# Optimization experiments

Hardware: AMD Instinct MI355X
Metric: run time of the kernel (lower is better)

## Reference

```python
import jax, jax.numpy as jnp
import numpy as np

B, L, DIM = 2, 2048, 512
HEADS, R, W, EH, T = 8, 8, 4, 16, 2
HD = DIM // HEADS  # 64
ROPE_BASE = 10000.0


def _local_window_edges(L, w):
    pos = np.arange(L)
    offs = np.concatenate([np.arange(-w, 0), np.arange(1, w + 1)])
    tg = pos[:, None] + offs[None, :]
    valid = (tg >= 0) & (tg < L)
    ii, _ = np.nonzero(valid)          # row-major, matches torch nonzero order
    return ii.astype(np.int32), tg[valid].astype(np.int32)


def setup_inputs() -> dict:
    key = jax.random.key(0)
    ks = jax.random.split(key, 12)
    sd = 0.02
    edge_i, edge_j = _local_window_edges(L, W)
    inp = {
        "x": jax.random.normal(ks[0], (B, L, DIM), jnp.float32),
        "edge_i": jnp.asarray(edge_i),
        "edge_j": jnp.asarray(edge_j),
        "te_w": jax.random.normal(ks[1], (DIM, DIM), jnp.float32) * sd,
        "te_b": jnp.zeros((DIM,), jnp.float32),
        "a1_w": jax.random.normal(ks[2], (2 * DIM, EH), jnp.float32) * sd,
        "a1_b": jnp.zeros((EH,), jnp.float32),
        "a2_w": jax.random.normal(ks[3], (EH, 1), jnp.float32) * sd,
        "a2_b": jnp.zeros((1,), jnp.float32),
        "l1_w": jax.random.normal(ks[4], (2 * DIM, EH), jnp.float32) * sd,
        "l1_b": jnp.zeros((EH,), jnp.float32),
        "l2_w": jax.random.normal(ks[5], (EH, HEADS * R * HD), jnp.float32) * sd,
        "l2_b": jnp.zeros((HEADS * R * HD,), jnp.float32),
        "step_sizes": jnp.full((T, L), -2.2, jnp.float32),
        "out_w": jax.random.normal(ks[6], (DIM, DIM), jnp.float32) * sd,
        "out_b": jnp.zeros((DIM,), jnp.float32),
    }
    return inp


def _rope_cos_sin(rel_pos):
    # rel_pos: [E] int -> cos/sin [E, HD] (rotate-half convention)
    inv_freq = 1.0 / (ROPE_BASE ** (jnp.arange(0, HD, 2, dtype=jnp.float32) / HD))
    ang = rel_pos.astype(jnp.float32)[:, None] * inv_freq[None, :]  # [E, HD/2]
    ang = jnp.concatenate([ang, ang], axis=-1)                      # [E, HD]
    return jnp.cos(ang), jnp.sin(ang)


def _rotate_half(x):
    x1, x2 = x[..., : HD // 2], x[..., HD // 2:]
    return jnp.concatenate([-x2, x1], axis=-1)


def reference(x, edge_i, edge_j, te_w, te_b, a1_w, a1_b, a2_w, a2_b,
              l1_w, l1_b, l2_w, l2_b, step_sizes, out_w, out_b):
    E = edge_i.shape[0]
    # token encoder -> heads: u [B, H, L, HD]
    u = (x @ te_w + te_b).reshape(B, L, HEADS, HD).transpose(0, 2, 1, 3)

    # edge features from raw x: [B, E, 2*DIM]
    ef = jnp.concatenate([x[:, edge_i], x[:, edge_j]], axis=-1)
    # alpha: softplus MLP -> [B, E]
    h = jax.nn.gelu(ef @ a1_w + a1_b, approximate=False)
    alphas = jax.nn.softplus((h @ a2_w + a2_b)[..., 0])
    # Lambda: MLP -> [B, E, H, R, HD], L2-normalized on last dim
    h2 = jax.nn.gelu(ef @ l1_w + l1_b, approximate=False)
    Lam = (h2 @ l2_w + l2_b).reshape(B, E, HEADS, R, HD)
    Lam = Lam / jnp.maximum(jnp.linalg.norm(Lam, axis=-1, keepdims=True), 1e-12)

    cos, sin = _rope_cos_sin(edge_i - edge_j)  # [E, HD] each

    for t in range(T):
        eta = jax.nn.softplus(step_sizes[t])[None, None, :, None]  # [1,1,L,1]
        u_i = u[:, :, edge_i]                                      # [B,H,E,HD]
        u_j = u[:, :, edge_j]
        u_i = u_i * cos + _rotate_half(u_i) * sin
        diff = u_i - u_j
        ld = jnp.einsum('behrd,bhed->bher', Lam, diff)
        residual = alphas[:, None, :, None] * diff + jnp.einsum('bher,behrd->bhed', ld, Lam)
        upd = jnp.zeros_like(u).at[:, :, edge_i, :].add(residual)
        upd = upd.at[:, :, edge_j, :].add(-residual)
        u = u - eta * upd

    u = u.transpose(0, 2, 1, 3).reshape(B, L, DIM)
    return u @ out_w + out_b
```

## Files before the change

kernel.cpp:

```cpp
#include <hip/hip_runtime.h>
#include <hip/hip_bf16.h>

#define B_   2
#define L_   2048
#define DIM_ 512
#define NH_  8
#define HD_  64
#define R_   8
#define EH_  16
#define T_   2

typedef unsigned int uint32;
typedef unsigned short ushort_t;

__device__ __forceinline__ float gelu_f(float x){
  return 0.5f * x * (1.0f + erff(x * 0.70710678118654752f));
}
__device__ __forceinline__ float softplus_f(float x){
  return (x > 20.f) ? x : log1pf(expf(x));
}
__device__ __forceinline__ constexpr int off_of(int o){ return (o < 4) ? o - 4 : o - 3; }
__device__ __forceinline__ ushort_t fbf(float f){
  uint32 u = __float_as_uint(f);
  return (ushort_t)((u + 0x7FFFu + ((u >> 16) & 1u)) >> 16);
}
__device__ __forceinline__ float blo(uint32 w){ return __uint_as_float(w << 16); }
__device__ __forceinline__ float bhi(uint32 w){ return __uint_as_float(w & 0xFFFF0000u); }

__global__ __launch_bounds__(256) void k_misc(
    const float* __restrict__ l2w, const float* __restrict__ l2b,
    const float* __restrict__ step,
    float* __restrict__ W2, float* __restrict__ eta,
    float* __restrict__ ropeC, float* __restrict__ ropeS,
    int* __restrict__ esrc, int* __restrict__ edst)
{
  int idx = blockIdx.x * 256 + threadIdx.x;
  if (idx < NH_*144*64){
    int d = idx & 63;
    int n = (idx >> 6) % 144;
    int h = idx / (144*64);
    int k = n >> 3, r = n & 7;
    int col = h*512 + r*64 + d;
    float v = 0.f;
    if (k < 16) v = l2w[k*4096 + col];
    else if (k == 16) v = l2b[col];
    W2[idx] = v;
    return;
  }
  idx -= NH_*144*64;
  if (idx < T_*L_){ eta[idx] = softplus_f(step[idx]); return; }
  idx -= T_*L_;
  if (idx < 9*32){
    int d = idx & 31, rel = (idx >> 5) - 4;
    float invf = expf(-((float)d / 32.f) * 9.210340371976184f);
    float ang = (float)rel * invf;
    ropeC[idx] = cosf(ang); ropeS[idx] = sinf(ang);
    return;
  }
  idx -= 9*32;
  if (idx < 2*8*L_){
    if (idx < 8*L_) esrc[idx] = -1; else edst[idx - 8*L_] = -1;
    return;
  }
}

__global__ __launch_bounds__(256) void k_cvtw(
    const float* __restrict__ W2, ushort_t* __restrict__ W2h)
{
  int idx = blockIdx.x * 256 + threadIdx.x;
  if (idx < NH_*144*64) W2h[idx] = fbf(W2[idx]);
}

__global__ __launch_bounds__(256) void k_gram(
    const float* __restrict__ W2, float* __restrict__ Gram)
{
  int idx = blockIdx.x * 256 + threadIdx.x;
  if (idx >= 8*8*17*17) return;
  int bq = idx % 17;
  int a  = (idx / 17) % 17;
  int r  = (idx / 289) & 7;
  int h  = idx / (289*8);
  const float* wa = W2 + ((size_t)(h*144 + a*8 + r))*64;
  const float* wb = W2 + ((size_t)(h*144 + bq*8 + r))*64;
  float s = 0.f;
  #pragma unroll 8
  for (int d = 0; d < 64; d++) s = fmaf(wa[d], wb[d], s);
  Gram[idx] = s;
}

__global__ __launch_bounds__(256) void k_fill(
    const int* __restrict__ ei, const int* __restrict__ ej, int E,
    int* __restrict__ esrc, int* __restrict__ edst)
{
  int e = blockIdx.x * 256 + threadIdx.x;
  if (e >= E) return;
  int i = ei[e], j = ej[e];
  int o = j - i;
  int slot = (o < 0) ? (o + 4) : (o + 3);
  esrc[slot*L_ + i] = e;
  edst[slot*L_ + j] = e;
}

__global__ __launch_bounds__(256) void k_te(
    const float* __restrict__ x, const float* __restrict__ w,
    const float* __restrict__ bias, float* __restrict__ u)
{
  __shared__ float As[16][64];
  __shared__ float Bs[16][64];
  const int m0 = blockIdx.x * 64;
  const int n0 = blockIdx.y * 64;
  const int tid = threadIdx.x;
  const int ty = tid >> 4, tx = tid & 15;
  float acc[4][4] = {};
  for (int k0 = 0; k0 < 512; k0 += 16){
    {
      int m = tid >> 2, seg = tid & 3;
      float4 v = *(const float4*)(x + (size_t)(m0 + m)*512 + k0 + seg*4);
      As[seg*4+0][m] = v.x; As[seg*4+1][m] = v.y;
      As[seg*4+2][m] = v.z; As[seg*4+3][m] = v.w;
    }
    {
      int k = tid >> 4, c = (tid & 15)*4;
      float4 v = *(const float4*)(w + (size_t)(k0 + k)*512 + n0 + c);
      *(float4*)&Bs[k][c] = v;
    }
    __syncthreads();
    #pragma unroll
    for (int k = 0; k < 16; k++){
      float4 a = *(const float4*)(&As[k][ty*4]);
      float4 b = *(const float4*)(&Bs[k][tx*4]);
      float av[4] = {a.x, a.y, a.z, a.w};
      float bv[4] = {b.x, b.y, b.z, b.w};
      #pragma unroll
      for (int ii = 0; ii < 4; ii++)
        #pragma unroll
        for (int jj = 0; jj < 4; jj++)
          acc[ii][jj] = fmaf(av[ii], bv[jj], acc[ii][jj]);
    }
    __syncthreads();
  }
  const int bb = m0 >> 11;
  const int lb = (m0 & 2047) + ty*4;
  #pragma unroll
  for (int jj = 0; jj < 4; jj++){
    int n = n0 + tx*4 + jj;
    float bv = bias[n];
    float4 o;
    o.x = acc[0][jj] + bv; o.y = acc[1][jj] + bv;
    o.z = acc[2][jj] + bv; o.w = acc[3][jj] + bv;
    *(float4*)&u[((size_t)(bb*512 + n))*2048 + lb] = o;
  }
}

__global__ __launch_bounds__(256) void k_pq(
    const float* __restrict__ x, const float* __restrict__ a1w,
    const float* __restrict__ l1w, float* __restrict__ PQ)
{
  __shared__ float As[16][64];
  __shared__ float Bs[16][64];
  const int m0 = blockIdx.x * 64;
  const int tid = threadIdx.x;
  const int ty = tid >> 4, tx = tid & 15;
  const int c = (tid & 15) * 4;
  const int group = c >> 4;
  const float* src = (group & 2) ? l1w : a1w;
  const int krow_off = (group & 1) ? 512 : 0;
  const int cc = c & 15;
  float acc[4][4] = {};
  for (int k0 = 0; k0 < 512; k0 += 16){
    {
      int m = tid >> 2, seg = tid & 3;
      float4 v = *(const float4*)(x + (size_t)(m0 + m)*512 + k0 + seg*4);
      As[seg*4+0][m] = v.x; As[seg*4+1][m] = v.y;
      As[seg*4+2][m] = v.z; As[seg*4+3][m] = v.w;
    }
    {
      int k = tid >> 4;
      float4 v = *(const float4*)(src + (size_t)(krow_off + k0 + k)*16 + cc);
      *(float4*)&Bs[k][c] = v;
    }
    __syncthreads();
    #pragma unroll
    for (int k = 0; k < 16; k++){
      float4 a = *(const float4*)(&As[k][ty*4]);
      float4 b = *(const float4*)(&Bs[k][tx*4]);
      float av[4] = {a.x, a.y, a.z, a.w};
      float bv[4] = {b.x, b.y, b.z, b.w};
      #pragma unroll
      for (int ii = 0; ii < 4; ii++)
        #pragma unroll
        for (int jj = 0; jj < 4; jj++)
          acc[ii][jj] = fmaf(av[ii], bv[jj], acc[ii][jj]);
    }
    __syncthreads();
  }
  #pragma unroll
  for (int ii = 0; ii < 4; ii++){
    int m = m0 + ty*4 + ii;
    float4 o;
    o.x = acc[ii][0]; o.y = acc[ii][1]; o.z = acc[ii][2]; o.w = acc[ii][3];
    *(float4*)&PQ[(size_t)m*64 + tx*4] = o;
  }
}

__global__ __launch_bounds__(256) void k_feat2(
    const float* __restrict__ PQ, const int* __restrict__ ei, const int* __restrict__ ej,
    const float* __restrict__ a1b, const float* __restrict__ a2w,
    const float* __restrict__ a2b, const float* __restrict__ l1b,
    int E, float* __restrict__ alphas, float* __restrict__ h2e,
    float* __restrict__ h2t)
{
  int e = blockIdx.x * 256 + threadIdx.x;
  int b = blockIdx.y;
  if (e >= E) return;
  int i = ei[e], j = ej[e];
  const float* Pi = PQ + ((size_t)b*L_ + i)*64;
  const float* Pj = PQ + ((size_t)b*L_ + j)*64;
  float ha[16], hl[16];
  #pragma unroll
  for (int q = 0; q < 4; q++){
    float4 p1 = *(const float4*)(Pi + q*4);
    float4 q1 = *(const float4*)(Pj + 16 + q*4);
    float4 p2 = *(const float4*)(Pi + 32 + q*4);
    float4 q2 = *(const float4*)(Pj + 48 + q*4);
    ha[q*4+0] = p1.x + q1.x; ha[q*4+1] = p1.y + q1.y;
    ha[q*4+2] = p1.z + q1.z; ha[q*4+3] = p1.w + q1.w;
    hl[q*4+0] = p2.x + q2.x; hl[q*4+1] = p2.y + q2.y;
    hl[q*4+2] = p2.z + q2.z; hl[q*4+3] = p2.w + q2.w;
  }
  float av = a2b[0];
  #pragma unroll
  for (int n = 0; n < 16; n++){
    float g = gelu_f(ha[n] + a1b[n]);
    av += g * a2w[n];
  }
  alphas[(size_t)b*E + e] = softplus_f(av);
  float* he = h2e + ((size_t)b*E + e)*16;
  #pragma unroll
  for (int n = 0; n < 16; n++){
    float g = gelu_f(hl[n] + l1b[n]);
    he[n] = g;
    h2t[((size_t)b*16 + n)*E + e] = g;
  }
}

__global__ __launch_bounds__(256) void k_norm(
    const float* __restrict__ Gram, const float* __restrict__ h2e,
    int E, float* __restrict__ ivsq)
{
  __shared__ float Gl[8*289];
  __shared__ float Hl[256*17];
  const int tid = threadIdx.x;
  const int bh = blockIdx.y;
  const int b = bh >> 3, h = bh & 7;
  const int eb = blockIdx.x*256;
  for (int it = tid; it < 2312; it += 256) Gl[it] = Gram[(size_t)h*2312 + it];
  {
    int ge = eb + tid;
    const float* hp = h2e + ((size_t)b*E + (ge < E ? ge : 0))*16;
    #pragma unroll
    for (int q = 0; q < 4; q++){
      float4 v = *(const float4*)(hp + q*4);
      Hl[tid*17+q*4+0]=v.x; Hl[tid*17+q*4+1]=v.y;
      Hl[tid*17+q*4+2]=v.z; Hl[tid*17+q*4+3]=v.w;
    }
    Hl[tid*17+16] = 1.f;
  }
  __syncthreads();
  int ge = eb + tid;
  if (ge >= E) return;
  float m17[17];
  #pragma unroll
  for (int k = 0; k < 17; k++) m17[k] = Hl[tid*17+k];
  float* ig = ivsq + ((size_t)bh*E + ge)*8;
  #pragma unroll
  for (int r = 0; r < 8; r++){
    float ss = 0.f;
    for (int a = 0; a < 17; a++){
      float ma = Hl[tid*17 + a];
      const float* Gr = Gl + r*289 + a*17;
      float inner = 0.f;
      #pragma unroll
      for (int bq = 0; bq < 17; bq++)
        inner = fmaf(m17[bq], Gr[bq], inner);
      ss = fmaf(ma, inner, ss);
    }
    ig[r] = 1.f / fmaxf(ss, 1e-24f);
  }
}

__global__ __launch_bounds__(256) void k_S(
    const float* __restrict__ u, const ushort_t* __restrict__ W2h,
    const float* __restrict__ h2t,
    const float* __restrict__ ropeC, const float* __restrict__ ropeS,
    const int* __restrict__ ei, const int* __restrict__ ej,
    int E, const float* __restrict__ ivsq, float* __restrict__ coefg)
{
  __shared__ uint32 Wl[136*32];
  __shared__ float rCT[288], rST[288];
  const int tid = threadIdx.x;
  const int bh = blockIdx.y;
  const int b = bh >> 3, h = bh & 7;
  const int eb = blockIdx.x*256;

  {
    const uint4* Wg4 = (const uint4*)(W2h + (size_t)h*144*64);
    for (int fi = tid; fi < 1088; fi += 256)
      ((uint4*)Wl)[fi] = Wg4[fi];
  }
  for (int it = tid; it < 288; it += 256){
    int rix = it >> 5, p = it & 31;
    rCT[p*9 + rix] = ropeC[it];
    rST[p*9 + rix] = ropeS[it];
  }
  __syncthreads();

  const int dq = tid & 3;
  const int qd = tid >> 2;
  const int e0 = eb + qd*4;
  const int p0 = 8*dq;
  const float* ub = u + ((size_t)(b*512 + h*64))*2048;
  const float* h2b = h2t + (size_t)b*16*E;

  int iiv[4], jjv[4], rxv[4];
  #pragma unroll
  for (int s = 0; s < 4; s++){
    int ge = e0 + s;
    int gi = (ge < E) ? ge : (E-1);
    iiv[s] = ei[gi]; jjv[s] = ej[gi];
    rxv[s] = iiv[s] - jjv[s] + 4;
  }

  float dA[4][8], dB[4][8];
  #pragma unroll
  for (int s = 0; s < 4; s++){
    #pragma unroll
    for (int q = 0; q < 8; q++){
      int dp = p0 + q;
      float c  = rCT[dp*9 + rxv[s]];
      float sn = rST[dp*9 + rxv[s]];
      float ui0 = ub[(size_t)dp*2048 + iiv[s]];
      float ui1 = ub[(size_t)(dp+32)*2048 + iiv[s]];
      float uj0 = ub[(size_t)dp*2048 + jjv[s]];
      float uj1 = ub[(size_t)(dp+32)*2048 + jjv[s]];
      dA[s][q] = ui0*c - ui1*sn - uj0;
      dB[s][q] = ui1*c + ui0*sn - uj1;
    }
  }

  const uint4* Wl4 = (const uint4*)Wl;
  float P[4][8] = {};
  for (int k = 0; k < 17; k++){
    float mk0, mk1, mk2, mk3;
    if (k < 16){
      float4 m4 = *(const float4*)(h2b + (size_t)k*E + e0);
      mk0 = m4.x; mk1 = m4.y; mk2 = m4.z; mk3 = m4.w;
    } else {
      mk0 = mk1 = mk2 = mk3 = 1.f;
    }
    const int rowb = (k*8)*8;
    #pragma unroll
    for (int r = 0; r < 8; r++){
      uint4 wa = Wl4[rowb + r*8 + dq];
      uint4 wb = Wl4[rowb + r*8 + 4 + dq];
      #pragma unroll
      for (int s = 0; s < 4; s++){
        float pd;
        pd = dA[s][0]*blo(wa.x);
        pd = fmaf(dA[s][1], bhi(wa.x), pd);
        pd = fmaf(dA[s][2], blo(wa.y), pd);
        pd = fmaf(dA[s][3], bhi(wa.y), pd);
        pd = fmaf(dA[s][4], blo(wa.z), pd);
        pd = fmaf(dA[s][5], bhi(wa.z), pd);
        pd = fmaf(dA[s][6], blo(wa.w), pd);
        pd = fmaf(dA[s][7], bhi(wa.w), pd);
        pd = fmaf(dB[s][0], blo(wb.x), pd);
        pd = fmaf(dB[s][1], bhi(wb.x), pd);
        pd = fmaf(dB[s][2], blo(wb.y), pd);
        pd = fmaf(dB[s][3], bhi(wb.y), pd);
        pd = fmaf(dB[s][4], blo(wb.z), pd);
        pd = fmaf(dB[s][5], bhi(wb.z), pd);
        pd = fmaf(dB[s][6], blo(wb.w), pd);
        pd = fmaf(dB[s][7], bhi(wb.w), pd);
        float mk = (s==0)?mk0:(s==1)?mk1:(s==2)?mk2:mk3;
        P[s][r] = fmaf(mk, pd, P[s][r]);
      }
    }
  }

  #pragma unroll
  for (int s = 0; s < 4; s++)
    #pragma unroll
    for (int r = 0; r < 8; r++){
      float v = P[s][r];
      v += __shfl_xor(v, 1);
      v += __shfl_xor(v, 2);
      P[s][r] = v;
    }

  int ge = e0 + dq;
  if (ge < E){
    float S8[8];
    #pragma unroll
    for (int r = 0; r < 8; r++){
      float v0 = P[0][r], v1 = P[1][r], v2 = P[2][r], v3 = P[3][r];
      S8[r] = (dq==0) ? v0 : (dq==1) ? v1 : (dq==2) ? v2 : v3;
    }
    const float* ig = ivsq + ((size_t)bh*E + ge)*8;
    float* cg = coefg + ((size_t)bh*E + ge)*8;
    #pragma unroll
    for (int r = 0; r < 8; r++) cg[r] = ig[r]*S8[r];
  }
}

__global__ __launch_bounds__(256) void k_apply(
    const float* __restrict__ uin, float* __restrict__ uout,
    const float* __restrict__ W2,
    const float* __restrict__ h2e, const float* __restrict__ coefg,
    const float* __restrict__ alphas,
    const float* __restrict__ ropeC, const float* __restrict__ ropeS,
    const int* __restrict__ esrc, const int* __restrict__ edst,
    const int* __restrict__ ei, const int* __restrict__ ej,
    const float* __restrict__ eta, int E, int t)
{
  __shared__ float smem[10816];
  float* Al  = smem;
  float* UtF = smem;
  float* SaF = smem + 4896;
  int*   Es  = (int*)(smem + 9216);
  float* rCl = smem + 10240;
  float* rSl = smem + 10528;

  const int tid = threadIdx.x;
  const int l0 = blockIdx.x * 64;
  const int bh = blockIdx.y;
  const int b = bh >> 3, h = bh & 7;
  const float* ub = uin + ((size_t)(b*512 + h*64))*2048;
  float*       uo = uout + ((size_t)(b*512 + h*64))*2048;
  const float* Wg = W2 + (size_t)h*144*64;

  #pragma unroll
  for (int it = 0; it < 4; it++){
    int si = it*256 + tid;
    int o = si >> 6, ll = si & 63;
    Es[si] = (o < 8) ? esrc[o*L_ + l0 + ll] : edst[(o-8)*L_ + l0 + ll];
  }
  for (int it = tid; it < 288; it += 256){ rCl[it] = ropeC[it]; rSl[it] = ropeS[it]; }
  for (int it = tid; it < 9216; it += 256) Al[it] = 0.f;
  __syncthreads();

  {
    const int l = tid & 63;
    const int kc = tid >> 6;
    const int kbase = kc*4;
    float areg[5][8];
    #pragma unroll
    for (int k = 0; k < 5; k++)
      #pragma unroll
      for (int r = 0; r < 8; r++) areg[k][r] = 0.f;
    for (int o = 0; o < 16; o++){
      int e = Es[o*64 + l];
      if (e < 0) continue;
      float sign = (o < 8) ? 1.f : -1.f;
      const float* hp = h2e + ((size_t)b*E + e)*16;
      const float* cp = coefg + ((size_t)bh*E + e)*8;
      float4 m4 = *(const float4*)(hp + kbase);
      float4 c0 = *(const float4*)cp;
      float4 c1 = *(const float4*)(cp + 4);
      float cf[8] = {c0.x, c0.y, c0.z, c0.w, c1.x, c1.y, c1.z, c1.w};
      float smv[4] = {sign*m4.x, sign*m4.y, sign*m4.z, sign*m4.w};
      #pragma unroll
      for (int k = 0; k < 4; k++)
        #pragma unroll
        for (int r = 0; r < 8; r++)
          areg[k][r] = fmaf(smv[k], cf[r], areg[k][r]);
      if (kc == 3){
        #pragma unroll
        for (int r = 0; r < 8; r++) areg[4][r] += sign*cf[r];
      }
    }
    const int sw = (l >> 2) & 3;
    #pragma unroll
    for (int k = 0; k < 4; k++){
      #pragma unroll
      for (int r = 0; r < 8; r++){
        int n = (kbase + k)*8 + r;
        Al[l*144 + (((n >> 2) ^ sw) << 2) + (n & 3)] = areg[k][r];
      }
    }
    if (kc == 3){
      #pragma unroll
      for (int r = 0; r < 8; r++){
        int n = 128 + r;
        Al[l*144 + (((n >> 2) ^ sw) << 2) + (n & 3)] = areg[4][r];
      }
    }
  }
  __syncthreads();

  const int lg = tid & 15, dg = tid >> 4;
  float acc[4][4] = {};
  {
    const int swr = lg & 3;
    for (int nf4 = 0; nf4 < 34; nf4++){
      int sf4 = (nf4 ^ swr) << 2;
      float4 Av[4];
      #pragma unroll
      for (int tt = 0; tt < 4; tt++)
        Av[tt] = *(const float4*)&Al[(lg*4 + tt)*144 + sf4];
      int n = nf4*4;
      #pragma unroll
      for (int q = 0; q < 4; q++){
        float4 wb = *(const float4*)(Wg + (size_t)(n + q)*64 + dg*4);
        #pragma unroll
        for (int tt = 0; tt < 4; tt++){
          float a = (q==0)?Av[tt].x:(q==1)?Av[tt].y:(q==2)?Av[tt].z:Av[tt].w;
          acc[tt][0] = fmaf(a, wb.x, acc[tt][0]);
          acc[tt][1] = fmaf(a, wb.y, acc[tt][1]);
          acc[tt][2] = fmaf(a, wb.z, acc[tt][2]);
          acc[tt][3] = fmaf(a, wb.w, acc[tt][3]);
        }
      }
    }
  }
  __syncthreads();

  #pragma unroll
  for (int it = 0; it < 18; it++){
    int flat = it*256 + tid;
    int d = flat / 72;
    int c = flat - d*72;
    int col = l0 - 4 + c;
    col = (col < 0) ? 0 : ((col > 2047) ? 2047 : col);
    UtF[c*68 + d] = ub[(size_t)d*2048 + col];
  }
  #pragma unroll
  for (int it = 0; it < 4; it++){
    int si = it*256 + tid;
    int e = Es[si];
    SaF[si] = (e >= 0) ? alphas[(size_t)b*E + e] : 0.f;
  }
  __syncthreads();

  const int pbase = (dg*4) & 31;
  const float sgn = (dg < 8) ? -1.f : 1.f;
  const int pcol = (dg*4 + 32) & 63;
  float4 rcv[8], rsv[8];
  #pragma unroll
  for (int o = 0; o < 8; o++){
    const int rix = 4 - off_of(o);
    rcv[o] = *(const float4*)&rCl[rix*32 + pbase];
    rsv[o] = *(const float4*)&rSl[rix*32 + pbase];
  }
  #pragma unroll
  for (int tt = 0; tt < 4; tt++){
    const int ll = lg*4 + tt;
    const int myl = l0 + ll;
    const int lrel = ll + 4;
    const float et = eta[t*L_ + myl];
    float4 ul  = *(const float4*)&UtF[lrel*68 + dg*4];
    float4 ulp = *(const float4*)&UtF[lrel*68 + pcol];
    float upd[4] = {acc[tt][0], acc[tt][1], acc[tt][2], acc[tt][3]};
    float ulv[4] = {ul.x, ul.y, ul.z, ul.w};
    float ulpv[4] = {ulp.x, ulp.y, ulp.z, ulp.w};
    #pragma unroll
    for (int o = 0; o < 8; o++){
      int e = Es[o*64 + ll];
      if (e >= 0){
        float al = SaF[o*64 + ll];
        float4 uj = *(const float4*)&UtF[(lrel + off_of(o))*68 + dg*4];
        float ujv[4] = {uj.x, uj.y, uj.z, uj.w};
        float rc[4] = {rcv[o].x, rcv[o].y, rcv[o].z, rcv[o].w};
        float rs[4] = {rsv[o].x, rsv[o].y, rsv[o].z, rsv[o].w};
        #pragma unroll
        for (int q = 0; q < 4; q++){
          float rope = rc[q]*ulv[q] + sgn*rs[q]*ulpv[q];
          upd[q] = fmaf(al, rope - ujv[q], upd[q]);
        }
      }
    }
    #pragma unroll
    for (int o = 0; o < 8; o++){
      int e = Es[(8 + o)*64 + ll];
      if (e >= 0){
        float al = SaF[(8 + o)*64 + ll];
        int lr2 = lrel - off_of(o);
        float4 ui  = *(const float4*)&UtF[lr2*68 + dg*4];
        float4 uip = *(const float4*)&UtF[lr2*68 + pcol];
        float uiv[4] = {ui.x, ui.y, ui.z, ui.w};
        float uipv[4] = {uip.x, uip.y, uip.z, uip.w};
        float rc[4] = {rcv[o].x, rcv[o].y, rcv[o].z, rcv[o].w};
        float rs[4] = {rsv[o].x, rsv[o].y, rsv[o].z, rsv[o].w};
        #pragma unroll
        for (int q = 0; q < 4; q++){
          float rope = rc[q]*uiv[q] + sgn*rs[q]*uipv[q];
          upd[q] -= al * (rope - ulv[q]);
        }
      }
    }
    #pragma unroll
    for (int q = 0; q < 4; q++)
      uo[(size_t)(dg*4 + q)*2048 + myl] = ulv[q] - et*upd[q];
  }
}

__global__ __launch_bounds__(256) void k_out(
    const float* __restrict__ u, const float* __restrict__ w,
    const float* __restrict__ bias, float* __restrict__ outp)
{
  __shared__ float As[16][64];
  __shared__ float Bs[16][64];
  const int m0 = blockIdx.x * 64;
  const int n0 = blockIdx.y * 64;
  const int tid = threadIdx.x;
  const int ty = tid >> 4, tx = tid & 15;
  const int bb = m0 >> 11;
  const int l0 = m0 & 2047;
  float acc[4][4] = {};
  for (int k0 = 0; k0 < 512; k0 += 16){
    {
      int k = tid >> 4, ls = (tid & 15)*4;
      float4 v = *(const float4*)&u[((size_t)(bb*512 + k0 + k))*2048 + l0 + ls];
      *(float4*)&As[k][ls] = v;
    }
    {
      int k = tid >> 4, c = (tid & 15)*4;
      float4 v = *(const float4*)(w + (size_t)(k0 + k)*512 + n0 + c);
      *(float4*)&Bs[k][c] = v;
    }
    __syncthreads();
    #pragma unroll
    for (int k = 0; k < 16; k++){
      float4 a = *(const float4*)(&As[k][ty*4]);
      float4 b = *(const float4*)(&Bs[k][tx*4]);
      float av[4] = {a.x, a.y, a.z, a.w};
      float bv[4] = {b.x, b.y, b.z, b.w};
      #pragma unroll
      for (int ii = 0; ii < 4; ii++)
        #pragma unroll
        for (int jj = 0; jj < 4; jj++)
          acc[ii][jj] = fmaf(av[ii], bv[jj], acc[ii][jj]);
    }
    __syncthreads();
  }
  float bv[4];
  #pragma unroll
  for (int jj = 0; jj < 4; jj++) bv[jj] = bias[n0 + tx*4 + jj];
  #pragma unroll
  for (int ii = 0; ii < 4; ii++){
    int l = l0 + ty*4 + ii;
    float4 o;
    o.x = acc[ii][0] + bv[0];
    o.y = acc[ii][1] + bv[1];
    o.z = acc[ii][2] + bv[2];
    o.w = acc[ii][3] + bv[3];
    *(float4*)&outp[((size_t)(bb*2048 + l))*512 + n0 + tx*4] = o;
  }
}

extern "C" void kernel_launch(void* const* d_in, const int* in_sizes, int n_in,
                              void* d_out, int out_size, void* d_ws, size_t ws_size,
                              hipStream_t stream)
{
  const float* x    = (const float*)d_in[0];
  const int*   ei   = (const int*)d_in[1];
  const int*   ej   = (const int*)d_in[2];
  const float* tew  = (const float*)d_in[3];
  const float* teb  = (const float*)d_in[4];
  const float* a1w  = (const float*)d_in[5];
  const float* a1b  = (const float*)d_in[6];
  const float* a2w  = (const float*)d_in[7];
  const float* a2b  = (const float*)d_in[8];
  const float* l1w  = (const float*)d_in[9];
  const float* l1b  = (const float*)d_in[10];
  const float* l2w  = (const float*)d_in[11];
  const float* l2b  = (const float*)d_in[12];
  const float* step = (const float*)d_in[13];
  const float* ow   = (const float*)d_in[14];
  const float* ob   = (const float*)d_in[15];
  float* outp = (float*)d_out;
  const int E = in_sizes[1];

  char* p = (char*)d_ws;
  auto carve = [&](size_t nbytes)->char*{
    char* q = p; p += (nbytes + 255) & ~(size_t)255; return q;
  };
  float* u0     = (float*)carve((size_t)B_*512*2048*4);
  float* u1     = (float*)carve((size_t)B_*512*2048*4);
  float* PQ     = (float*)carve((size_t)B_*L_*64*4);
  float* h2e    = (float*)carve((size_t)B_*E*16*4);
  float* h2t    = (float*)carve((size_t)(B_*16*E + 64)*4);
  float* alphas = (float*)carve((size_t)B_*E*4);
  float* coefg  = (float*)carve((size_t)B_*NH_*E*8*4);
  float* ivsq   = (float*)carve((size_t)B_*NH_*E*8*4);
  float* W2     = (float*)carve((size_t)NH_*144*64*4);
  ushort_t* W2h = (ushort_t*)carve((size_t)NH_*144*64*2);
  float* Gram   = (float*)carve((size_t)8*8*17*17*4);
  float* eta    = (float*)carve((size_t)T_*L_*4);
  float* ropeC  = (float*)carve((size_t)288*4);
  float* ropeS  = (float*)carve((size_t)288*4);
  int*   esrc   = (int*)carve((size_t)8*L_*4);
  int*   edst   = (int*)carve((size_t)8*L_*4);

  {
    int total = NH_*144*64 + T_*L_ + 9*32 + 2*8*L_;
    k_misc<<<dim3((total + 255)/256), dim3(256), 0, stream>>>(
        l2w, l2b, step, W2, eta, ropeC, ropeS, esrc, edst);
  }
  k_cvtw<<<dim3((NH_*144*64 + 255)/256), dim3(256), 0, stream>>>(W2, W2h);
  k_gram<<<dim3((8*8*17*17 + 255)/256), dim3(256), 0, stream>>>(W2, Gram);
  k_fill<<<dim3((E + 255)/256), dim3(256), 0, stream>>>(ei, ej, E, esrc, edst);
  k_te<<<dim3(64, 8), dim3(256), 0, stream>>>(x, tew, teb, u0);
  k_pq<<<dim3(64), dim3(256), 0, stream>>>(x, a1w, l1w, PQ);
  k_feat2<<<dim3((E + 255)/256, B_), dim3(256), 0, stream>>>(
      PQ, ei, ej, a1b, a2w, a2b, l1b, E, alphas, h2e, h2t);

  k_norm<<<dim3((E + 255)/256, B_*NH_), dim3(256), 0, stream>>>(Gram, h2e, E, ivsq);

  const int etiles = (E + 255)/256;
  float* ucur = u0;
  float* unxt = u1;
  for (int t = 0; t < T_; t++){
    k_S<<<dim3(etiles, B_*NH_), dim3(256), 0, stream>>>(
        ucur, W2h, h2t, ropeC, ropeS, ei, ej, E, ivsq, coefg);
    k_apply<<<dim3(L_/64, B_*NH_), dim3(256), 0, stream>>>(
        ucur, unxt, W2, h2e, coefg, alphas, ropeC, ropeS,
        esrc, edst, ei, ej, eta, E, t);
    float* tmp = ucur; ucur = unxt; unxt = tmp;
  }

  k_out<<<dim3(64, 8), dim3(256), 0, stream>>>(ucur, ow, ob, outp);
}
```

Baseline: 377.9 us.

## Split k_S dot products across 8 lanes with paired bf16 weight layout

The bf16 weight table is repacked so each 32-bit word holds the rotate-half pair (d, d+32), letting one uint4 LDS load feed both halves of the rope-rotated diff. k_S now uses 8 lanes per edge group, each handling 4 of the 32 rotary pairs, instead of 4 lanes with 8 pairs each. Each block therefore covers 128 edges and the grid doubles. This lowers per-thread registers and LDS loads and raises parallelism, at the cost of an extra shuffle-reduction step, idle lanes during the final store, and twice as many block-level weight staging loads.

```diff
diff --git a/kernel.cpp b/kernel.cpp
--- a/kernel.cpp
+++ b/kernel.cpp
@@ -65,10 +65,17 @@
 }
 
 __global__ __launch_bounds__(256) void k_cvtw(
-    const float* __restrict__ W2, ushort_t* __restrict__ W2h)
+    const float* __restrict__ W2, uint32* __restrict__ W2p)
 {
   int idx = blockIdx.x * 256 + threadIdx.x;
-  if (idx < NH_*144*64) W2h[idx] = fbf(W2[idx]);
+  if (idx >= NH_*144*32) return;
+  int dp = idx & 31;
+  int n  = (idx >> 5) % 144;
+  int h  = idx / (144*32);
+  const float* row = W2 + ((size_t)h*144 + n)*64;
+  uint32 lo = fbf(row[dp]);
+  uint32 hi = fbf(row[dp+32]);
+  W2p[idx] = lo | (hi << 16);
 }
 
 __global__ __launch_bounds__(256) void k_gram(
@@ -290,7 +297,7 @@
 }
 
 __global__ __launch_bounds__(256) void k_S(
-    const float* __restrict__ u, const ushort_t* __restrict__ W2h,
+    const float* __restrict__ u, const uint32* __restrict__ W2p,
     const float* __restrict__ h2t,
     const float* __restrict__ ropeC, const float* __restrict__ ropeS,
     const int* __restrict__ ei, const int* __restrict__ ej,
@@ -301,10 +308,10 @@
   const int tid = threadIdx.x;
   const int bh = blockIdx.y;
   const int b = bh >> 3, h = bh & 7;
-  const int eb = blockIdx.x*256;
+  const int eb = blockIdx.x*128;
 
   {
-    const uint4* Wg4 = (const uint4*)(W2h + (size_t)h*144*64);
+    const uint4* Wg4 = (const uint4*)(W2p + (size_t)h*144*32);
     for (int fi = tid; fi < 1088; fi += 256)
       ((uint4*)Wl)[fi] = Wg4[fi];
   }
@@ -315,10 +322,10 @@
   }
   __syncthreads();
 
-  const int dq = tid & 3;
-  const int qd = tid >> 2;
+  const int og = tid & 7;
+  const int qd = tid >> 3;
   const int e0 = eb + qd*4;
-  const int p0 = 8*dq;
+  const int p0 = og*4;
   const float* ub = u + ((size_t)(b*512 + h*64))*2048;
   const float* h2b = h2t + (size_t)b*16*E;
 
@@ -331,11 +338,11 @@
     rxv[s] = iiv[s] - jjv[s] + 4;
   }
 
-  float dA[4][8], dB[4][8];
+  float dA[4][4], dB[4][4];
   #pragma unroll
   for (int s = 0; s < 4; s++){
     #pragma unroll
-    for (int q = 0; q < 8; q++){
+    for (int q = 0; q < 4; q++){
       int dp = p0 + q;
       float c  = rCT[dp*9 + rxv[s]];
       float sn = rST[dp*9 + rxv[s]];
@@ -361,27 +368,22 @@
     const int rowb = (k*8)*8;
     #pragma unroll
     for (int r = 0; r < 8; r++){
-      uint4 wa = Wl4[rowb + r*8 + dq];
-      uint4 wb = Wl4[rowb + r*8 + 4 + dq];
+      uint4 w = Wl4[rowb + r*8 + og];
+      float wa0 = blo(w.x), wb0 = bhi(w.x);
+      float wa1 = blo(w.y), wb1 = bhi(w.y);
+      float wa2 = blo(w.z), wb2 = bhi(w.z);
+      float wa3 = blo(w.w), wb3 = bhi(w.w);
       #pragma unroll
       for (int s = 0; s < 4; s++){
         float pd;
-        pd = dA[s][0]*blo(wa.x);
-        pd = fmaf(dA[s][1], bhi(wa.x), pd);
-        pd = fmaf(dA[s][2], blo(wa.y), pd);
-        pd = fmaf(dA[s][3], bhi(wa.y), pd);
-        pd = fmaf(dA[s][4], blo(wa.z), pd);
-        pd = fmaf(dA[s][5], bhi(wa.z), pd);
-        pd = fmaf(dA[s][6], blo(wa.w), pd);
-        pd = fmaf(dA[s][7], bhi(wa.w), pd);
-        pd = fmaf(dB[s][0], blo(wb.x), pd);
-        pd = fmaf(dB[s][1], bhi(wb.x), pd);
-        pd = fmaf(dB[s][2], blo(wb.y), pd);
-        pd = fmaf(dB[s][3], bhi(wb.y), pd);
-        pd = fmaf(dB[s][4], blo(wb.z), pd);
-        pd = fmaf(dB[s][5], bhi(wb.z), pd);
-        pd = fmaf(dB[s][6], blo(wb.w), pd);
-        pd = fmaf(dB[s][7], bhi(wb.w), pd);
+        pd = dA[s][0]*wa0;
+        pd = fmaf(dB[s][0], wb0, pd);
+        pd = fmaf(dA[s][1], wa1, pd);
+        pd = fmaf(dB[s][1], wb1, pd);
+        pd = fmaf(dA[s][2], wa2, pd);
+        pd = fmaf(dB[s][2], wb2, pd);
+        pd = fmaf(dA[s][3], wa3, pd);
+        pd = fmaf(dB[s][3], wb3, pd);
         float mk = (s==0)?mk0:(s==1)?mk1:(s==2)?mk2:mk3;
         P[s][r] = fmaf(mk, pd, P[s][r]);
       }
@@ -395,21 +397,24 @@
       float v = P[s][r];
       v += __shfl_xor(v, 1);
       v += __shfl_xor(v, 2);
+      v += __shfl_xor(v, 4);
       P[s][r] = v;
     }
 
-  int ge = e0 + dq;
-  if (ge < E){
-    float S8[8];
-    #pragma unroll
-    for (int r = 0; r < 8; r++){
-      float v0 = P[0][r], v1 = P[1][r], v2 = P[2][r], v3 = P[3][r];
-      S8[r] = (dq==0) ? v0 : (dq==1) ? v1 : (dq==2) ? v2 : v3;
-    }
-    const float* ig = ivsq + ((size_t)bh*E + ge)*8;
-    float* cg = coefg + ((size_t)bh*E + ge)*8;
-    #pragma unroll
-    for (int r = 0; r < 8; r++) cg[r] = ig[r]*S8[r];
+  if (og < 4){
+    int ge = e0 + og;
+    if (ge < E){
+      float S8[8];
+      #pragma unroll
+      for (int r = 0; r < 8; r++){
+        float v0 = P[0][r], v1 = P[1][r], v2 = P[2][r], v3 = P[3][r];
+        S8[r] = (og==0) ? v0 : (og==1) ? v1 : (og==2) ? v2 : v3;
+      }
+      const float* ig = ivsq + ((size_t)bh*E + ge)*8;
+      float* cg = coefg + ((size_t)bh*E + ge)*8;
+      #pragma unroll
+      for (int r = 0; r < 8; r++) cg[r] = ig[r]*S8[r];
+    }
   }
 }
 
@@ -694,7 +699,7 @@
   float* coefg  = (float*)carve((size_t)B_*NH_*E*8*4);
   float* ivsq   = (float*)carve((size_t)B_*NH_*E*8*4);
   float* W2     = (float*)carve((size_t)NH_*144*64*4);
-  ushort_t* W2h = (ushort_t*)carve((size_t)NH_*144*64*2);
+  uint32* W2p   = (uint32*)carve((size_t)NH_*144*32*4);
   float* Gram   = (float*)carve((size_t)8*8*17*17*4);
   float* eta    = (float*)carve((size_t)T_*L_*4);
   float* ropeC  = (float*)carve((size_t)288*4);
@@ -707,7 +712,7 @@
     k_misc<<<dim3((total + 255)/256), dim3(256), 0, stream>>>(
         l2w, l2b, step, W2, eta, ropeC, ropeS, esrc, edst);
   }
-  k_cvtw<<<dim3((NH_*144*64 + 255)/256), dim3(256), 0, stream>>>(W2, W2h);
+  k_cvtw<<<dim3((NH_*144*32 + 255)/256), dim3(256), 0, stream>>>(W2, W2p);
   k_gram<<<dim3((8*8*17*17 + 255)/256), dim3(256), 0, stream>>>(W2, Gram);
   k_fill<<<dim3((E + 255)/256), dim3(256), 0, stream>>>(ei, ej, E, esrc, edst);
   k_te<<<dim3(64, 8), dim3(256), 0, stream>>>(x, tew, teb, u0);
@@ -717,12 +722,12 @@
 
   k_norm<<<dim3((E + 255)/256, B_*NH_), dim3(256), 0, stream>>>(Gram, h2e, E, ivsq);
 
-  const int etiles = (E + 255)/256;
+  const int etiles = (E + 127)/128;
   float* ucur = u0;
   float* unxt = u1;
   for (int t = 0; t < T_; t++){
     k_S<<<dim3(etiles, B_*NH_), dim3(256), 0, stream>>>(
-        ucur, W2h, h2t, ropeC, ropeS, ei, ej, E, ivsq, coefg);
+        ucur, W2p, h2t, ropeC, ropeS, ei, ej, E, ivsq, coefg);
     k_apply<<<dim3(L_/64, B_*NH_), dim3(256), 0, stream>>>(
         ucur, unxt, W2, h2e, coefg, alphas, ropeC, ropeS,
         esrc, edst, ei, ej, eta, E, t);
```

Measured after the change: 380.5 us. No clear change (+0.7%).
